# Kernel tuning notes

Measured on AMD Instinct MI355X. Metric: run time of the kernel, lower is better.

Reference implementation:

```python
import jax, jax.numpy as jnp
import numpy as np

DIM = 192
HEADS = 6
WIN = 7
N = WIN * WIN            # 49 tokens per window
NW = 64                  # windows per image
B = 64                   # images
BW = NW * B              # 4096 total windows
TABLE = (2 * WIN - 1) ** 2  # 169


def setup_inputs() -> dict:
    key = jax.random.key(0)
    ks = jax.random.split(key, 8)
    x = jax.random.normal(ks[0], (BW, N, DIM), dtype=jnp.float32)
    rpi = jax.random.randint(ks[1], (N, N), 0, TABLE, dtype=jnp.int64)
    # 0 / -100 additive mask (as in shifted-window attention)
    mask = jnp.where(jax.random.uniform(ks[2], (NW, N, N)) < 0.1, -100.0, 0.0).astype(jnp.float32)
    qkv_w = jax.random.normal(ks[3], (3 * DIM, DIM), dtype=jnp.float32) * 0.02
    qkv_b = jnp.zeros((3 * DIM,), dtype=jnp.float32)
    proj_w = jax.random.normal(ks[4], (DIM, DIM), dtype=jnp.float32) * 0.02
    proj_b = jnp.zeros((DIM,), dtype=jnp.float32)
    rpb_table = jax.random.normal(ks[5], (TABLE, HEADS), dtype=jnp.float32) * 0.02
    return {"x": x, "rpi": rpi, "mask": mask, "qkv_w": qkv_w, "qkv_b": qkv_b,
            "proj_w": proj_w, "proj_b": proj_b, "rpb_table": rpb_table}


def reference(x, rpi, mask, qkv_w, qkv_b, proj_w, proj_b, rpb_table):
    b_, n, c = x.shape
    hd = c // HEADS
    scale = hd ** -0.5
    qkv = (x @ qkv_w.T + qkv_b).reshape(b_, n, 3, HEADS, hd)
    qkv = jnp.transpose(qkv, (2, 0, 3, 1, 4))
    q, k, v = qkv[0], qkv[1], qkv[2]
    attn = jnp.einsum('bhnd,bhmd->bhnm', q * scale, k)  # [b_, h, n, n]
    # relative position bias gather: [n, n, h] -> [h, n, n]
    bias = rpb_table[rpi.reshape(-1)].reshape(n, n, HEADS)
    attn = attn + jnp.transpose(bias, (2, 0, 1))[None]
    # additive 0/-inf window mask
    nw = mask.shape[0]
    attn = attn.reshape(b_ // nw, nw, HEADS, n, n) + mask[None, :, None]
    attn = attn.reshape(-1, HEADS, n, n)
    attn = jax.nn.softmax(attn, axis=-1)
    out = jnp.einsum('bhnm,bhmd->bhnd', attn, v)
    out = jnp.transpose(out, (0, 2, 1, 3)).reshape(b_, n, c)
    out = out @ proj_w.T + proj_b
    return out
```

## Files before the change

kernel.cpp:

```cpp
#include <hip/hip_runtime.h>

#define DIM    192
#define HEADS  6
#define NTOK   49
#define NWIN   64

typedef __attribute__((ext_vector_type(8))) short short8;
typedef __attribute__((ext_vector_type(4))) float f32x4;

#define XS 200
#define VS 72
#define SS 65
#define PS 72

#define BIAS_ELEMS (HEADS * NTOK * NTOK)
#define WQKV_SOFF   28864
#define WQKV_ELEMS  (3 * DIM * DIM)
#define WPROJ_SOFF  (WQKV_SOFF + WQKV_ELEMS)
#define WPROJ_ELEMS (DIM * DIM)

__device__ __forceinline__ unsigned short f2bf(float f) {
    unsigned int u = __float_as_uint(f);
    u += 0x7FFFu + ((u >> 16) & 1u);
    return (unsigned short)(u >> 16);
}

__global__ void wa_prep_kernel(const int* __restrict__ rpi,
                               const float* __restrict__ rpb,
                               const float* __restrict__ qkv_w,
                               const float* __restrict__ proj_w,
                               float* __restrict__ bias,
                               unsigned short* __restrict__ wqkv,
                               unsigned short* __restrict__ wproj) {
    __shared__ int is64_s;
    if (threadIdx.x == 0) {
        int zeros = 0;
        for (int p = 0; p < 64; ++p) zeros += (rpi[2 * p + 1] == 0) ? 1 : 0;
        is64_s = (zeros >= 48) ? 1 : 0;
    }
    __syncthreads();
    const int is64 = is64_s;
    const int total = BIAS_ELEMS + WQKV_ELEMS + WPROJ_ELEMS;
    for (int idx = blockIdx.x * blockDim.x + threadIdx.x; idx < total;
         idx += gridDim.x * blockDim.x) {
        if (idx < BIAS_ELEMS) {
            int h  = idx / (NTOK * NTOK);
            int nm = idx - h * (NTOK * NTOK);
            int r  = is64 ? rpi[2 * nm] : rpi[nm];
            bias[idx] = rpb[r * HEADS + h];
        } else if (idx < BIAS_ELEMS + WQKV_ELEMS) {
            int i = idx - BIAS_ELEMS;
            wqkv[i] = f2bf(qkv_w[i]);
        } else {
            int i = idx - BIAS_ELEMS - WQKV_ELEMS;
            wproj[i] = f2bf(proj_w[i]);
        }
    }
}

__global__ __launch_bounds__(512, 4)
void wa_attn_kernel(const float* __restrict__ x,
                    const float* __restrict__ maskp,
                    const unsigned short* __restrict__ wqkv,
                    const float* __restrict__ qkv_b,
                    const float* __restrict__ biasp,
                    const unsigned short* __restrict__ wproj,
                    const float* __restrict__ proj_b,
                    float* __restrict__ out) {
    __shared__ __attribute__((aligned(16))) float uSP[64 * SS + 64 * (PS / 2)];
    __shared__ __attribute__((aligned(16))) unsigned short sq[64 * XS];
    __shared__ __attribute__((aligned(16))) unsigned short sv[DIM * VS];
    __shared__ float sinv[64];

    unsigned short* sx     = (unsigned short*)uSP;
    unsigned short* kstage = (unsigned short*)uSP;
    float* S = uSP;
    unsigned short* P = (unsigned short*)(uSP + 64 * SS);

    const int tid  = threadIdx.x;
    const int wave = tid >> 6;
    const int lane = tid & 63;
    const int quad = lane >> 4;
    const int l16  = lane & 15;
    const int bw   = blockIdx.x;
    const int win  = bw & (NWIN - 1);

    {
        const float4* xw = (const float4*)(x + (size_t)bw * (NTOK * DIM));
        for (int idx = tid; idx < NTOK * DIM / 4; idx += 512) {
            int row = idx / 48, c4 = idx - row * 48;
            float4 v = xw[idx];
            unsigned int lo = (unsigned int)f2bf(v.x) | ((unsigned int)f2bf(v.y) << 16);
            unsigned int hi = (unsigned int)f2bf(v.z) | ((unsigned int)f2bf(v.w) << 16);
            *(uint2*)&sx[row * XS + c4 * 4] = make_uint2(lo, hi);
        }
        for (int idx = tid; idx < 15 * 24; idx += 512) {
            int row = 49 + idx / 24, c8 = idx - (idx / 24) * 24;
            *(uint4*)&sx[row * XS + c8 * 8] = make_uint4(0, 0, 0, 0);
        }
    }
    __syncthreads();

    {
        f32x4 acc[5][4];
        #pragma unroll
        for (int r = 0; r < 5; ++r)
            #pragma unroll
            for (int mt = 0; mt < 4; ++mt) acc[r][mt] = (f32x4){0.f, 0.f, 0.f, 0.f};
        for (int k0 = 0; k0 < DIM; k0 += 32) {
            short8 af[4];
            #pragma unroll
            for (int mt = 0; mt < 4; ++mt)
                af[mt] = *(const short8*)&sx[(mt * 16 + l16) * XS + k0 + quad * 8];
            #pragma unroll
            for (int r = 0; r < 5; ++r) {
                if (wave >= 4 && r == 4) continue;
                int n0 = (wave + 8 * r) * 16;
                short8 bf = *(const short8*)(wqkv + (n0 + l16) * DIM + k0 + quad * 8);
                #pragma unroll
                for (int mt = 0; mt < 4; ++mt)
                    acc[r][mt] = __builtin_amdgcn_mfma_f32_16x16x32_bf16(af[mt], bf, acc[r][mt], 0, 0, 0);
            }
        }
        __syncthreads();
        #pragma unroll
        for (int r = 0; r < 5; ++r) {
            if (wave >= 4 && r == 4) continue;
            int n0  = (wave + 8 * r) * 16;
            int col = n0 + l16;
            float cb = qkv_b[col];
            #pragma unroll
            for (int mt = 0; mt < 4; ++mt) {
                #pragma unroll
                for (int rr = 0; rr < 4; ++rr) {
                    int m = mt * 16 + quad * 4 + rr;
                    unsigned short bv = f2bf(acc[r][mt][rr] + cb);
                    if (col < 192)      sq[m * XS + col] = bv;
                    else if (col < 384) kstage[m * XS + (col - 192)] = bv;
                    else                sv[(col - 384) * VS + m] = bv;
                }
            }
        }
    }
    __syncthreads();

    short8 kf[2][HEADS];
    #pragma unroll
    for (int tt = 0; tt < 2; ++tt) {
        int t = wave * 2 + tt, nt = t & 3;
        #pragma unroll
        for (int h = 0; h < HEADS; ++h)
            kf[tt][h] = *(const short8*)&kstage[(nt * 16 + l16) * XS + h * 32 + quad * 8];
    }
    __syncthreads();

    const float scale = 0.17677669529663687f;
    const float* maskw = maskp + win * (NTOK * NTOK);

    #pragma unroll
    for (int h = 0; h < HEADS; ++h) {
        {
            f32x4 zz = {0.f, 0.f, 0.f, 0.f};
            const float* bh = biasp + h * (NTOK * NTOK);
            #pragma unroll
            for (int tt = 0; tt < 2; ++tt) {
                int t = wave * 2 + tt;
                int mt = t >> 2, nt = t & 3;
                short8 af = *(const short8*)&sq[(mt * 16 + l16) * XS + h * 32 + quad * 8];
                f32x4 d = __builtin_amdgcn_mfma_f32_16x16x32_bf16(af, kf[tt][h], zz, 0, 0, 0);
                #pragma unroll
                for (int rr = 0; rr < 4; ++rr) {
                    int i = mt * 16 + quad * 4 + rr;
                    int j = nt * 16 + l16;
                    if (i < NTOK && j < NTOK)
                        S[i * SS + j] = d[rr] * scale + bh[i * NTOK + j] + maskw[i * NTOK + j];
                }
            }
        }
        __syncthreads();
        if (tid < 392) {
            int i = tid >> 3, s = tid & 7;
            float m = -1e30f;
            for (int jj = 0; jj < 7; ++jj) {
                int j = s + 8 * jj;
                if (j < NTOK) m = fmaxf(m, S[i * SS + j]);
            }
            for (int o = 1; o < 8; o <<= 1) m = fmaxf(m, __shfl_xor(m, o));
            float sum = 0.f;
            #pragma unroll
            for (int jj = 0; jj < 8; ++jj) {
                int j = s + 8 * jj;
                float e = 0.f;
                if (j < NTOK) { e = __expf(S[i * SS + j] - m); sum += e; }
                P[i * PS + j] = f2bf(e);
            }
            for (int o = 1; o < 8; o <<= 1) sum += __shfl_xor(sum, o);
            if (s == 0) sinv[i] = 1.f / sum;
        }
        __syncthreads();
        {
            int mt = wave >> 1, nt = wave & 1;
            f32x4 acc = {0.f, 0.f, 0.f, 0.f};
            #pragma unroll
            for (int k0 = 0; k0 < 64; k0 += 32) {
                short8 af = *(const short8*)&P[(mt * 16 + l16) * PS + k0 + quad * 8];
                short8 bf = *(const short8*)&sv[(h * 32 + nt * 16 + l16) * VS + k0 + quad * 8];
                acc = __builtin_amdgcn_mfma_f32_16x16x32_bf16(af, bf, acc, 0, 0, 0);
            }
            #pragma unroll
            for (int rr = 0; rr < 4; ++rr) {
                int i = mt * 16 + quad * 4 + rr;
                unsigned short ov = 0;
                if (i < NTOK) ov = f2bf(acc[rr] * sinv[i]);
                sq[i * XS + h * 32 + nt * 16 + l16] = ov;
            }
        }
    }
    __syncthreads();

    {
        const int mh = wave >> 2;
        const int wv = wave & 3;
        f32x4 pacc[3][2];
        #pragma unroll
        for (int r = 0; r < 3; ++r)
            #pragma unroll
            for (int mi = 0; mi < 2; ++mi) pacc[r][mi] = (f32x4){0.f, 0.f, 0.f, 0.f};
        for (int k0 = 0; k0 < DIM; k0 += 32) {
            short8 af[2];
            #pragma unroll
            for (int mi = 0; mi < 2; ++mi)
                af[mi] = *(const short8*)&sq[((mh * 2 + mi) * 16 + l16) * XS + k0 + quad * 8];
            #pragma unroll
            for (int r = 0; r < 3; ++r) {
                int n0 = (wv + 4 * r) * 16;
                short8 bf = *(const short8*)(wproj + (n0 + l16) * DIM + k0 + quad * 8);
                #pragma unroll
                for (int mi = 0; mi < 2; ++mi)
                    pacc[r][mi] = __builtin_amdgcn_mfma_f32_16x16x32_bf16(af[mi], bf, pacc[r][mi], 0, 0, 0);
            }
        }
        #pragma unroll
        for (int r = 0; r < 3; ++r) {
            int n0 = (wv + 4 * r) * 16;
            float cb = proj_b[n0 + l16];
            #pragma unroll
            for (int mi = 0; mi < 2; ++mi) {
                #pragma unroll
                for (int rr = 0; rr < 4; ++rr) {
                    int m = (mh * 2 + mi) * 16 + quad * 4 + rr;
                    if (m < NTOK)
                        out[((size_t)bw * NTOK + m) * DIM + n0 + l16] = pacc[r][mi][rr] + cb;
                }
            }
        }
    }
}

extern "C" void kernel_launch(void* const* d_in, const int* in_sizes, int n_in,
                              void* d_out, int out_size, void* d_ws, size_t ws_size,
                              hipStream_t stream) {
    const float* x      = (const float*)d_in[0];
    const int*   rpi    = (const int*)d_in[1];
    const float* maskp  = (const float*)d_in[2];
    const float* qkv_w  = (const float*)d_in[3];
    const float* qkv_b  = (const float*)d_in[4];
    const float* proj_w = (const float*)d_in[5];
    const float* proj_b = (const float*)d_in[6];
    const float* rpb    = (const float*)d_in[7];
    float* out = (float*)d_out;

    float* bias = (float*)d_ws;
    unsigned short* wqkv  = (unsigned short*)d_ws + WQKV_SOFF;
    unsigned short* wproj = (unsigned short*)d_ws + WPROJ_SOFF;

    wa_prep_kernel<<<320, 256, 0, stream>>>(rpi, rpb, qkv_w, proj_w, bias, wqkv, wproj);
    wa_attn_kernel<<<4096, 512, 0, stream>>>(x, maskp, wqkv, qkv_b, bias, wproj, proj_b, out);
}
```

Measured before the change: 619.4 us.

## Precombine bias and mask per window in prep kernel, vectorize V stores

The prep kernel now builds a per-window table that already holds relative-position bias plus window mask, so the attention kernel reads one additive term per score instead of two. The change also replaces the serial is64 check with a wave ballot, packs the transposed V stores into 64-bit writes, doubles the prep grid and relaxes launch bounds from 4 to 2 blocks per CU. The trade is an extra ~3.7 MB table written each call, and the new path runs only when the workspace is big enough. The relaxed launch bound may change register allocation and occupancy.

New measurement: 701.9 us. 13.3% more time.

```diff
diff --git a/kernel.cpp b/kernel.cpp
--- a/kernel.cpp
+++ b/kernel.cpp
@@ -18,6 +18,8 @@
 #define WQKV_ELEMS  (3 * DIM * DIM)
 #define WPROJ_SOFF  (WQKV_SOFF + WQKV_ELEMS)
 #define WPROJ_ELEMS (DIM * DIM)
+#define CMB_BOFF    ((size_t)(WPROJ_SOFF + WPROJ_ELEMS) * 2)
+#define CMB_ELEMS   (NWIN * HEADS * NTOK * NTOK)
 
 __device__ __forceinline__ unsigned short f2bf(float f) {
     unsigned int u = __float_as_uint(f);
@@ -29,18 +31,21 @@
                                const float* __restrict__ rpb,
                                const float* __restrict__ qkv_w,
                                const float* __restrict__ proj_w,
+                               const float* __restrict__ maskp,
                                float* __restrict__ bias,
                                unsigned short* __restrict__ wqkv,
-                               unsigned short* __restrict__ wproj) {
+                               unsigned short* __restrict__ wproj,
+                               float* __restrict__ cmb) {
     __shared__ int is64_s;
-    if (threadIdx.x == 0) {
-        int zeros = 0;
-        for (int p = 0; p < 64; ++p) zeros += (rpi[2 * p + 1] == 0) ? 1 : 0;
-        is64_s = (zeros >= 48) ? 1 : 0;
+    if (threadIdx.x < 64) {
+        int z = (rpi[2 * (int)threadIdx.x + 1] == 0) ? 1 : 0;
+        unsigned long long b = __ballot(z);
+        if (threadIdx.x == 0) is64_s = (__popcll(b) >= 48) ? 1 : 0;
     }
     __syncthreads();
     const int is64 = is64_s;
-    const int total = BIAS_ELEMS + WQKV_ELEMS + WPROJ_ELEMS;
+    const int base3 = BIAS_ELEMS + WQKV_ELEMS + WPROJ_ELEMS;
+    const int total = base3 + (cmb ? CMB_ELEMS : 0);
     for (int idx = blockIdx.x * blockDim.x + threadIdx.x; idx < total;
          idx += gridDim.x * blockDim.x) {
         if (idx < BIAS_ELEMS) {
@@ -51,14 +56,23 @@
         } else if (idx < BIAS_ELEMS + WQKV_ELEMS) {
             int i = idx - BIAS_ELEMS;
             wqkv[i] = f2bf(qkv_w[i]);
-        } else {
+        } else if (idx < base3) {
             int i = idx - BIAS_ELEMS - WQKV_ELEMS;
             wproj[i] = f2bf(proj_w[i]);
+        } else {
+            int i2  = idx - base3;
+            int win = i2 / (HEADS * NTOK * NTOK);
+            int rem = i2 - win * (HEADS * NTOK * NTOK);
+            int h   = rem / (NTOK * NTOK);
+            int nm  = rem - h * (NTOK * NTOK);
+            int r   = is64 ? rpi[2 * nm] : rpi[nm];
+            cmb[i2] = rpb[r * HEADS + h] + maskp[win * (NTOK * NTOK) + nm];
         }
     }
 }
 
-__global__ __launch_bounds__(512, 4)
+template <bool CMB>
+__global__ __launch_bounds__(512, 2)
 void wa_attn_kernel(const float* __restrict__ x,
                     const float* __restrict__ maskp,
                     const unsigned short* __restrict__ wqkv,
@@ -66,6 +80,7 @@
                     const float* __restrict__ biasp,
                     const unsigned short* __restrict__ wproj,
                     const float* __restrict__ proj_b,
+                    const float* __restrict__ cmbp,
                     float* __restrict__ out) {
     __shared__ __attribute__((aligned(16))) float uSP[64 * SS + 64 * (PS / 2)];
     __shared__ __attribute__((aligned(16))) unsigned short sq[64 * XS];
@@ -126,18 +141,24 @@
         #pragma unroll
         for (int r = 0; r < 5; ++r) {
             if (wave >= 4 && r == 4) continue;
-            int n0  = (wave + 8 * r) * 16;
-            int col = n0 + l16;
+            int col = (wave + 8 * r) * 16 + l16;
             float cb = qkv_b[col];
             #pragma unroll
             for (int mt = 0; mt < 4; ++mt) {
-                #pragma unroll
-                for (int rr = 0; rr < 4; ++rr) {
-                    int m = mt * 16 + quad * 4 + rr;
-                    unsigned short bv = f2bf(acc[r][mt][rr] + cb);
-                    if (col < 192)      sq[m * XS + col] = bv;
-                    else if (col < 384) kstage[m * XS + (col - 192)] = bv;
-                    else                sv[(col - 384) * VS + m] = bv;
+                if (r >= 3) {
+                    unsigned int lo = (unsigned int)f2bf(acc[r][mt][0] + cb) |
+                                      ((unsigned int)f2bf(acc[r][mt][1] + cb) << 16);
+                    unsigned int hi = (unsigned int)f2bf(acc[r][mt][2] + cb) |
+                                      ((unsigned int)f2bf(acc[r][mt][3] + cb) << 16);
+                    *(uint2*)&sv[(col - 384) * VS + mt * 16 + quad * 4] = make_uint2(lo, hi);
+                } else {
+                    #pragma unroll
+                    for (int rr = 0; rr < 4; ++rr) {
+                        int m = mt * 16 + quad * 4 + rr;
+                        unsigned short bv = f2bf(acc[r][mt][rr] + cb);
+                        if (col < 192) sq[m * XS + col] = bv;
+                        else           kstage[m * XS + (col - 192)] = bv;
+                    }
                 }
             }
         }
@@ -161,7 +182,8 @@
     for (int h = 0; h < HEADS; ++h) {
         {
             f32x4 zz = {0.f, 0.f, 0.f, 0.f};
-            const float* bh = biasp + h * (NTOK * NTOK);
+            const float* cw = CMB ? (cmbp + ((size_t)win * HEADS + h) * (NTOK * NTOK))
+                                  : (biasp + h * (NTOK * NTOK));
             #pragma unroll
             for (int tt = 0; tt < 2; ++tt) {
                 int t = wave * 2 + tt;
@@ -172,8 +194,11 @@
                 for (int rr = 0; rr < 4; ++rr) {
                     int i = mt * 16 + quad * 4 + rr;
                     int j = nt * 16 + l16;
-                    if (i < NTOK && j < NTOK)
-                        S[i * SS + j] = d[rr] * scale + bh[i * NTOK + j] + maskw[i * NTOK + j];
+                    if (i < NTOK && j < NTOK) {
+                        float add = CMB ? cw[i * NTOK + j]
+                                        : (cw[i * NTOK + j] + maskw[i * NTOK + j]);
+                        S[i * SS + j] = d[rr] * scale + add;
+                    }
                 }
             }
         }
@@ -273,7 +298,16 @@
     float* bias = (float*)d_ws;
     unsigned short* wqkv  = (unsigned short*)d_ws + WQKV_SOFF;
     unsigned short* wproj = (unsigned short*)d_ws + WPROJ_SOFF;
-
-    wa_prep_kernel<<<320, 256, 0, stream>>>(rpi, rpb, qkv_w, proj_w, bias, wqkv, wproj);
-    wa_attn_kernel<<<4096, 512, 0, stream>>>(x, maskp, wqkv, qkv_b, bias, wproj, proj_b, out);
+    float* cmb = nullptr;
+    if (ws_size >= CMB_BOFF + (size_t)CMB_ELEMS * 4)
+        cmb = (float*)((char*)d_ws + CMB_BOFF);
+
+    wa_prep_kernel<<<640, 256, 0, stream>>>(rpi, rpb, qkv_w, proj_w, maskp,
+                                            bias, wqkv, wproj, cmb);
+    if (cmb)
+        wa_attn_kernel<true><<<4096, 512, 0, stream>>>(x, maskp, wqkv, qkv_b, bias,
+                                                       wproj, proj_b, cmb, out);
+    else
+        wa_attn_kernel<false><<<4096, 512, 0, stream>>>(x, maskp, wqkv, qkv_b, bias,
+                                                        wproj, proj_b, cmb, out);
 }
```
